# Performance work log

Hardware: AMD Instinct MI355X
Metric: run time of the kernel (lower is better)

The kernel has to match this reference:

```python
import jax, jax.numpy as jnp
import numpy as np

B, S, D = 2, 2048, 1024
H, HK, HD = 16, 4, 64          # query heads, kv heads, head dim = D//H
WIN = 1024                     # sliding attention window
E, K, DH = 8, 2, 2048          # experts, top_k, expert hidden (== d_head ctor arg)
ATTN_EPS, FFN_EPS = 1e-5, 1e-6
ROPE_THETA = 10000.0


def setup_inputs() -> dict:
    key = jax.random.key(0)
    ks = jax.random.split(key, 9)
    sc = 0.02
    # real rotary frequencies for positions [start_pos, start_pos+S)
    start_pos = 0
    inv_freq = 1.0 / (ROPE_THETA ** (jnp.arange(0, HD, 2, dtype=jnp.float32) / HD))  # [HD//2]
    pos = jnp.arange(start_pos, start_pos + S, dtype=jnp.float32)
    ang = pos[:, None] * inv_freq[None, :]  # [S, HD//2]
    return {
        'x': jax.random.normal(ks[0], (B, S, D), jnp.float32),
        'freqs_cos': jnp.cos(ang),
        'freqs_sin': jnp.sin(ang),
        'attn_norm_w': jnp.ones((D,), jnp.float32),
        'wq': jax.random.normal(ks[1], (D, H * HD), jnp.float32) * sc,
        'wk': jax.random.normal(ks[2], (D, HK * HD), jnp.float32) * sc,
        'wv': jax.random.normal(ks[3], (D, HK * HD), jnp.float32) * sc,
        'wo': jax.random.normal(ks[4], (H * HD, D), jnp.float32) * sc,
        'ffn_norm_w': jnp.ones((D,), jnp.float32),
        'router_w': jax.random.normal(ks[5], (D, E), jnp.float32) * sc,
        'w1': jax.random.normal(ks[6], (E, D, DH), jnp.float32) * sc,
        'w2': jax.random.normal(ks[7], (E, DH, D), jnp.float32) * sc,
        'start_pos': start_pos,
    }


def _rmsnorm(x, w, eps):
    return x * jax.lax.rsqrt(jnp.mean(x * x, axis=-1, keepdims=True) + eps) * w


def _rope(t, cos, sin):
    # t: [B,S,N,HD]; cos/sin: [S,HD//2] -> complex rotation on consecutive pairs
    shp = t.shape
    t = t.reshape(shp[:-1] + (HD // 2, 2))
    t0, t1 = t[..., 0], t[..., 1]
    c = cos[None, :, None, :]
    s = sin[None, :, None, :]
    r = jnp.stack([t0 * c - t1 * s, t0 * s + t1 * c], axis=-1)
    return r.reshape(shp)


def reference(x, freqs_cos, freqs_sin, attn_norm_w, wq, wk, wv, wo,
              ffn_norm_w, router_w, w1, w2, start_pos):
    # ---- attention sublayer (RMSNorm -> GQA sliding-window attn) ----
    hn = _rmsnorm(x, attn_norm_w, ATTN_EPS)
    q = (hn @ wq).reshape(B, S, H, HD)
    k = (hn @ wk).reshape(B, S, HK, HD)
    v = (hn @ wv).reshape(B, S, HK, HD)
    q = _rope(q, freqs_cos, freqs_sin)
    k = _rope(k, freqs_cos, freqs_sin)
    rep = H // HK
    k = jnp.repeat(k, rep, axis=2)  # [B,S,H,HD]
    v = jnp.repeat(v, rep, axis=2)
    scale = 1.0 / np.sqrt(HD).astype(np.float32)
    scores = jnp.einsum('bqhd,bkhd->bhqk', q, k) * scale  # [B,H,S,S]
    qi = jnp.arange(S) + start_pos
    kj = jnp.arange(S) + start_pos
    mask = (kj[None, :] <= qi[:, None]) & (qi[:, None] - kj[None, :] < WIN)
    scores = jnp.where(mask[None, None], scores, jnp.float32(-1e30))
    attn = jax.nn.softmax(scores, axis=-1)
    o = jnp.einsum('bhqk,bkhd->bqhd', attn, v).reshape(B, S, H * HD)
    h = x + o @ wo

    # ---- MoE sublayer (RMSNorm -> router top-k -> expert FFNs) ----
    fn = _rmsnorm(h, ffn_norm_w, FFN_EPS).reshape(-1, D)  # [T,D], T=B*S
    probs = jax.nn.softmax(fn @ router_w, axis=-1)        # [T,E]
    top_vals, top_idx = jax.lax.top_k(probs, K)           # [T,K]
    gates = top_vals / jnp.sum(top_vals, axis=-1, keepdims=True)
    gmat = jnp.sum(jax.nn.one_hot(top_idx, E, dtype=fn.dtype) * gates[..., None], axis=1)  # [T,E]
    moe = jnp.zeros_like(fn)
    for e in range(E):  # fixed small expert count
        moe = moe + gmat[:, e:e + 1] * (jax.nn.silu(fn @ w1[e]) @ w2[e])
    return h + moe.reshape(B, S, D)
```

## Files before the change

kernel.cpp:

```cpp
#include <hip/hip_runtime.h>
#include <hip/hip_bf16.h>

using bf16 = __hip_bfloat16;
typedef __attribute__((ext_vector_type(8))) short bf16x8;
typedef __attribute__((ext_vector_type(4))) short short4v;
typedef __attribute__((ext_vector_type(4))) float f32x4;

#define DEV static __device__ __forceinline__

DEV float b2f(bf16 v) { return __bfloat162float(v); }
DEV bf16  f2b(float f) { return __float2bfloat16(f); }
DEV short bbits(float f) { bf16 h = __float2bfloat16(f); short u; __builtin_memcpy(&u, &h, 2); return u; }

#define GL2LDS(g, l)                                                        \
  __builtin_amdgcn_global_load_lds(                                         \
      (const __attribute__((address_space(1))) void*)(g),                   \
      (__attribute__((address_space(3))) void*)(l), 16, 0, 0)

__global__ __launch_bounds__(256) void transpose_convert(
    const float* __restrict__ src, bf16* __restrict__ dst, int K, int N) {
  __shared__ float tile[64][65];
  int n0 = blockIdx.x * 64, k0 = blockIdx.y * 64;
  size_t bo = (size_t)blockIdx.z * K * N;
  src += bo; dst += bo;
  int t = threadIdx.x;
  int rr = t >> 4, cc = (t & 15) * 4;
#pragma unroll
  for (int p = 0; p < 4; ++p) {
    int r = rr + p * 16;
    const float4 v = *(const float4*)&src[(size_t)(k0 + r) * N + n0 + cc];
    tile[r][cc] = v.x; tile[r][cc + 1] = v.y; tile[r][cc + 2] = v.z; tile[r][cc + 3] = v.w;
  }
  __syncthreads();
#pragma unroll
  for (int p = 0; p < 4; ++p) {
    int nr = rr + p * 16;
    short4v o;
    o[0] = bbits(tile[cc + 0][nr]);
    o[1] = bbits(tile[cc + 1][nr]);
    o[2] = bbits(tile[cc + 2][nr]);
    o[3] = bbits(tile[cc + 3][nr]);
    *(short4v*)&dst[(size_t)(n0 + nr) * K + k0 + cc] = o;
  }
}

__global__ __launch_bounds__(256) void rmsnorm_kernel(
    const float* __restrict__ x, const float* __restrict__ w,
    bf16* __restrict__ o, float eps) {
  int row = blockIdx.x;
  const float* xr = x + (size_t)row * 1024;
  int t = threadIdx.x;
  float4 v = *(const float4*)&xr[t * 4];
  float ss = v.x * v.x + v.y * v.y + v.z * v.z + v.w * v.w;
#pragma unroll
  for (int d = 32; d; d >>= 1) ss += __shfl_down(ss, d);
  __shared__ float red[4];
  if ((t & 63) == 0) red[t >> 6] = ss;
  __syncthreads();
  float sum = red[0] + red[1] + red[2] + red[3];
  float sc = rsqrtf(sum * (1.f / 1024.f) + eps);
  const float4 wv = *(const float4*)&w[t * 4];
  short4v pk;
  pk[0] = bbits(v.x * sc * wv.x);
  pk[1] = bbits(v.y * sc * wv.y);
  pk[2] = bbits(v.z * sc * wv.z);
  pk[3] = bbits(v.w * sc * wv.w);
  *(short4v*)&o[(size_t)row * 1024 + t * 4] = pk;
}

__global__ __launch_bounds__(256) void rope_kernel(
    bf16* __restrict__ tbuf, const float* __restrict__ fcos,
    const float* __restrict__ fsin, int ncols, int pshift) {
  int tid = blockIdx.x * 256 + threadIdx.x;
  int row = tid >> pshift;
  int cp = tid & ((1 << pshift) - 1);
  if (row >= 4096) return;
  int i = cp & 31;
  int s = row & 2047;
  bf16* p = tbuf + (size_t)row * ncols + cp * 2;
  float t0 = b2f(p[0]), t1 = b2f(p[1]);
  float c = fcos[s * 32 + i], sn = fsin[s * 32 + i];
  p[0] = f2b(t0 * c - t1 * sn);
  p[1] = f2b(t0 * sn + t1 * c);
}

template <int MODE>
__global__ __launch_bounds__(256) void gemm_bt(
    const bf16* __restrict__ A, const bf16* __restrict__ Bt,
    int M, int N, int Kd,
    bf16* __restrict__ outb, float* __restrict__ outf,
    const float* __restrict__ resid,
    const int* __restrict__ counts, const int* __restrict__ offsets,
    const int* __restrict__ tok, const int* __restrict__ slotl,
    const float* __restrict__ gatel,
    float* __restrict__ slot0, float* __restrict__ slot1) {
  int count = M, off = 0;
  const bf16* Ap = A;
  const bf16* Bp = Bt;
  if (MODE == 2 || MODE == 3) {
    int e = blockIdx.z;
    count = counts[e]; off = offsets[e];
    Bp = Bt + (size_t)e * Kd * N;
    if (MODE == 3) Ap = A + (size_t)off * Kd;
  }
  int mb = blockIdx.y * 128, nb = blockIdx.x * 128;
  if (mb >= count) return;

  __shared__ __align__(16) bf16 As[2][128 * 32];
  __shared__ __align__(16) bf16 Bs[2][128 * 32];

  int t = threadIdx.x;
  int lane = t & 63, wid = t >> 6;

  const bf16* agl[2];
  const bf16* bgl[2];
#pragma unroll
  for (int iss = 0; iss < 2; ++iss) {
    int p = iss * 256 + wid * 64 + lane;
    int row = p >> 2, cs = p & 3;
    int c = cs ^ (row & 3);
    int m = mb + row;
    const bf16* abase;
    if (MODE == 2) {
      int tokid = (m < count) ? tok[off + m] : 0;
      abase = A + (size_t)tokid * Kd;
    } else {
      int mm = (m < count) ? m : 0;
      abase = Ap + (size_t)mm * Kd;
    }
    agl[iss] = abase + c * 8;
    bgl[iss] = Bp + (size_t)(nb + row) * Kd + c * 8;
  }

  int wr = (wid >> 1) * 64, wc = (wid & 1) * 64;
  int lr = lane & 15, lkc = lane >> 4;

  auto stage = [&](int buf, int kt) {
#pragma unroll
    for (int iss = 0; iss < 2; ++iss) {
      GL2LDS(agl[iss] + kt * 32, &As[buf][(iss * 256 + wid * 64) * 8]);
      GL2LDS(bgl[iss] + kt * 32, &Bs[buf][(iss * 256 + wid * 64) * 8]);
    }
  };

  const f32x4 fzero = {0.f, 0.f, 0.f, 0.f};
  f32x4 acc[4][4];
#pragma unroll
  for (int i = 0; i < 4; ++i)
#pragma unroll
    for (int j = 0; j < 4; ++j) acc[i][j] = fzero;

  int nk = Kd >> 5;
  stage(0, 0);
  __syncthreads();
  for (int kt = 0; kt < nk; ++kt) {
    int cur = kt & 1;
    if (kt + 1 < nk) stage(cur ^ 1, kt + 1);
    bf16x8 af[4], bfr[4];
#pragma unroll
    for (int i = 0; i < 4; ++i) {
      int r = wr + i * 16 + lr;
      af[i] = *(const bf16x8*)&As[cur][r * 32 + ((lkc ^ (r & 3)) * 8)];
    }
#pragma unroll
    for (int j = 0; j < 4; ++j) {
      int r = wc + j * 16 + lr;
      bfr[j] = *(const bf16x8*)&Bs[cur][r * 32 + ((lkc ^ (r & 3)) * 8)];
    }
#pragma unroll
    for (int i = 0; i < 4; ++i)
#pragma unroll
      for (int j = 0; j < 4; ++j)
        acc[i][j] = __builtin_amdgcn_mfma_f32_16x16x32_bf16(af[i], bfr[j], acc[i][j], 0, 0, 0);
    __syncthreads();
  }

  int rq = lane >> 4;
#pragma unroll
  for (int i = 0; i < 4; ++i) {
#pragma unroll
    for (int j = 0; j < 4; ++j) {
      if (MODE == 4) {
        int n = nb + wc + j * 16 + lr;
        int kh = n >> 6, d = n & 63;
        int m0 = mb + wr + i * 16 + rq * 4;
        int bb = m0 >> 11, s = m0 & 2047;
        short4v pk;
#pragma unroll
        for (int r = 0; r < 4; ++r) pk[r] = bbits(acc[i][j][r]);
        *(short4v*)&outb[((size_t)((bb * 4 + kh) * 64 + d)) * 2048 + s] = pk;
      } else {
#pragma unroll
        for (int r = 0; r < 4; ++r) {
          int m = mb + wr + i * 16 + rq * 4 + r;
          int n = nb + wc + j * 16 + lr;
          float v = acc[i][j][r];
          if (MODE == 0) {
            outb[(size_t)m * N + n] = f2b(v);
          } else if (MODE == 1) {
            outf[(size_t)m * N + n] = resid[(size_t)m * N + n] + v;
          } else if (MODE == 2) {
            if (m < count) {
              float sg = 1.f / (1.f + expf(-v));
              outb[(size_t)(off + m) * N + n] = f2b(v * sg);
            }
          } else if (MODE == 3) {
            if (m < count) {
              int row = off + m;
              int tk = tok[row];
              float g = gatel[row];
              float* dst = slotl[row] ? slot1 : slot0;
              dst[(size_t)tk * N + n] = g * v;
            }
          }
        }
      }
    }
  }
}

__global__ __launch_bounds__(256) void attn_kernel(
    const bf16* __restrict__ q, const bf16* __restrict__ kb,
    const bf16* __restrict__ vt, bf16* __restrict__ o) {
  int qb = blockIdx.x, h = blockIdx.y, b = blockIdx.z;
  int kh = h >> 2;
  int t = threadIdx.x;
  int lane = t & 63, wid = t >> 6;
  int lr = lane & 15, lkc = lane >> 4;
  int q0 = qb * 64;
  int qrow = q0 + wid * 16;

  __shared__ __align__(16) bf16 Ks[64 * 64];
  __shared__ __align__(16) bf16 Vs[64 * 64];
  __shared__ __align__(16) bf16 Ps[4][16 * 72];

  bf16x8 aq[2];
#pragma unroll
  for (int kk = 0; kk < 2; ++kk)
    aq[kk] = *(const bf16x8*)&q[(size_t)(b * 2048 + qrow + lr) * 1024 + h * 64 + kk * 32 + lkc * 8];

  const f32x4 fzero = {0.f, 0.f, 0.f, 0.f};
  f32x4 oacc[4];
  float mrun[4], lrun[4];
#pragma unroll
  for (int r = 0; r < 4; ++r) { oacc[r] = fzero; mrun[r] = -1e30f; lrun[r] = 0.f; }

  int klo = q0 - 1023; if (klo < 0) klo = 0;
  int tlo = klo >> 6, thi = q0 >> 6;
  int skey = t >> 3;
  int sch = t & 7;

  for (int kt = tlo; kt <= thi; ++kt) {
    int kbase = kt * 64;
#pragma unroll
    for (int pp = 0; pp < 2; ++pp) {
      int key = skey + pp * 32;
      bf16x8 kv = *(const bf16x8*)&kb[(size_t)(b * 2048 + kbase + key) * 256 + kh * 64 + sch * 8];
      *(bf16x8*)&Ks[key * 64 + ((sch ^ (key & 7)) * 8)] = kv;
      bf16x8 vv = *(const bf16x8*)&vt[((size_t)((b * 4 + kh) * 64 + key)) * 2048 + kbase + sch * 8];
      *(bf16x8*)&Vs[key * 64 + ((sch ^ (key & 7)) * 8)] = vv;
    }
    __syncthreads();

    f32x4 sacc[4];
#pragma unroll
    for (int nt = 0; nt < 4; ++nt) sacc[nt] = fzero;
#pragma unroll
    for (int nt = 0; nt < 4; ++nt)
#pragma unroll
      for (int kk = 0; kk < 2; ++kk) {
        int r = nt * 16 + lr;
        bf16x8 bk = *(const bf16x8*)&Ks[r * 64 + (((kk * 4 + lkc) ^ (r & 7)) * 8)];
        sacc[nt] = __builtin_amdgcn_mfma_f32_16x16x32_bf16(aq[kk], bk, sacc[nt], 0, 0, 0);
      }

    float sval[4][4], mt[4];
    int qg = qrow + lkc * 4;
#pragma unroll
    for (int r = 0; r < 4; ++r) mt[r] = -1e30f;
#pragma unroll
    for (int nt = 0; nt < 4; ++nt) {
      int kkey = kbase + nt * 16 + lr;
#pragma unroll
      for (int r = 0; r < 4; ++r) {
        float s = sacc[nt][r] * 0.125f;
        int qq = qg + r;
        bool valid = (kkey <= qq) && (qq - kkey < 1024);
        s = valid ? s : -1e30f;
        sval[nt][r] = s;
        mt[r] = fmaxf(mt[r], s);
      }
    }
#pragma unroll
    for (int d = 1; d < 16; d <<= 1)
#pragma unroll
      for (int r = 0; r < 4; ++r) mt[r] = fmaxf(mt[r], __shfl_xor(mt[r], d));
    float alpha[4], rs[4];
#pragma unroll
    for (int r = 0; r < 4; ++r) {
      float mn = fmaxf(mrun[r], mt[r]);
      alpha[r] = __expf(mrun[r] - mn);
      mrun[r] = mn;
      rs[r] = 0.f;
    }
#pragma unroll
    for (int nt = 0; nt < 4; ++nt)
#pragma unroll
      for (int r = 0; r < 4; ++r) {
        float pv = __expf(sval[nt][r] - mrun[r]);
        sval[nt][r] = pv;
        rs[r] += pv;
      }
#pragma unroll
    for (int d = 1; d < 16; d <<= 1)
#pragma unroll
      for (int r = 0; r < 4; ++r) rs[r] += __shfl_xor(rs[r], d);
#pragma unroll
    for (int r = 0; r < 4; ++r) lrun[r] = lrun[r] * alpha[r] + rs[r];
#pragma unroll
    for (int dt = 0; dt < 4; ++dt) {
      f32x4 t4 = oacc[dt];
#pragma unroll
      for (int r = 0; r < 4; ++r) t4[r] *= alpha[r];
      oacc[dt] = t4;
    }

    bf16* pw = &Ps[wid][0];
#pragma unroll
    for (int nt = 0; nt < 4; ++nt)
#pragma unroll
      for (int r = 0; r < 4; ++r)
        pw[(lkc * 4 + r) * 72 + nt * 16 + lr] = f2b(sval[nt][r]);
    __syncthreads();

    bf16x8 pa[2];
#pragma unroll
    for (int kk2 = 0; kk2 < 2; ++kk2)
      pa[kk2] = *(const bf16x8*)&pw[lr * 72 + kk2 * 32 + lkc * 8];
#pragma unroll
    for (int dt = 0; dt < 4; ++dt)
#pragma unroll
      for (int kk2 = 0; kk2 < 2; ++kk2) {
        int rrow = dt * 16 + lr;
        bf16x8 bv = *(const bf16x8*)&Vs[rrow * 64 + (((kk2 * 4 + lkc) ^ (rrow & 7)) * 8)];
        oacc[dt] = __builtin_amdgcn_mfma_f32_16x16x32_bf16(pa[kk2], bv, oacc[dt], 0, 0, 0);
      }
    __syncthreads();
  }

#pragma unroll
  for (int dt = 0; dt < 4; ++dt)
#pragma unroll
    for (int r = 0; r < 4; ++r) {
      int qq = qrow + lkc * 4 + r;
      int dd = dt * 16 + lr;
      o[(size_t)(b * 2048 + qq) * 1024 + h * 64 + dd] = f2b(oacc[dt][r] / lrun[r]);
    }
}

__global__ __launch_bounds__(256) void router_kernel(
    const float* __restrict__ h, const float* __restrict__ ffnw,
    const float* __restrict__ rw, float* __restrict__ gates,
    int* __restrict__ eidx) {
  int wid = threadIdx.x >> 6, lane = threadIdx.x & 63;
  int row = blockIdx.x * 4 + wid;
  const float* hr = h + (size_t)row * 1024;
  float xs[16];
  float ss = 0.f;
#pragma unroll
  for (int i = 0; i < 16; ++i) { float f = hr[lane + i * 64]; xs[i] = f; ss += f * f; }
#pragma unroll
  for (int d = 32; d; d >>= 1) ss += __shfl_xor(ss, d);
  float sc = rsqrtf(ss * (1.f / 1024.f) + 1e-6f);
  float lg[8];
#pragma unroll
  for (int e = 0; e < 8; ++e) lg[e] = 0.f;
#pragma unroll
  for (int i = 0; i < 16; ++i) {
    int d = lane + i * 64;
    float f = xs[i] * sc * ffnw[d];
    const float* rr = rw + d * 8;
#pragma unroll
    for (int e = 0; e < 8; ++e) lg[e] += f * rr[e];
  }
#pragma unroll
  for (int d = 32; d; d >>= 1)
#pragma unroll
    for (int e = 0; e < 8; ++e) lg[e] += __shfl_xor(lg[e], d);
  if (lane == 0) {
    int e0 = 0; float v0 = lg[0];
#pragma unroll
    for (int e = 1; e < 8; ++e) if (lg[e] > v0) { v0 = lg[e]; e0 = e; }
    int e1 = -1; float v1 = -1e30f;
#pragma unroll
    for (int e = 0; e < 8; ++e) if (e != e0 && lg[e] > v1) { v1 = lg[e]; e1 = e; }
    float r1 = expf(v1 - v0);
    float den = 1.f + r1;
    gates[row * 2] = 1.f / den;
    gates[row * 2 + 1] = r1 / den;
    eidx[row * 2] = e0;
    eidx[row * 2 + 1] = e1;
  }
}

__global__ __launch_bounds__(1024) void moe_setup(
    const int* __restrict__ eidx, const float* __restrict__ gates,
    int* __restrict__ counts, int* __restrict__ offsets,
    int* __restrict__ tok, int* __restrict__ slotl, float* __restrict__ gatel) {
  __shared__ int hist[8];
  __shared__ int cur[8];
  int t = threadIdx.x;
  if (t < 8) hist[t] = 0;
  __syncthreads();
  int e[8];
#pragma unroll
  for (int c = 0; c < 8; ++c) {
    e[c] = eidx[c * 1024 + t];
    atomicAdd(&hist[e[c]], 1);
  }
  __syncthreads();
  if (t == 0) {
    int o = 0;
#pragma unroll
    for (int i = 0; i < 8; ++i) {
      offsets[i] = o; cur[i] = o;
      int cnt = hist[i]; counts[i] = cnt; o += cnt;
    }
  }
  __syncthreads();
#pragma unroll
  for (int c = 0; c < 8; ++c) {
    int i = c * 1024 + t;
    int pos = atomicAdd(&cur[e[c]], 1);
    tok[pos] = i >> 1;
    slotl[pos] = i & 1;
    gatel[pos] = gates[i];
  }
}

__global__ __launch_bounds__(256) void final_add(
    const float* __restrict__ h, const float* __restrict__ s0,
    const float* __restrict__ s1, float* __restrict__ out) {
  size_t i = ((size_t)blockIdx.x * 256 + threadIdx.x) * 4;
  float4 a = *(const float4*)&h[i];
  float4 b = *(const float4*)&s0[i];
  float4 c = *(const float4*)&s1[i];
  float4 o;
  o.x = a.x + b.x + c.x; o.y = a.y + b.y + c.y;
  o.z = a.z + b.z + c.z; o.w = a.w + b.w + c.w;
  *(float4*)&out[i] = o;
}

extern "C" void kernel_launch(void* const* d_in, const int* in_sizes, int n_in,
                              void* d_out, int out_size, void* d_ws, size_t ws_size,
                              hipStream_t stream) {
  const float* x    = (const float*)d_in[0];
  const float* fcos = (const float*)d_in[1];
  const float* fsin = (const float*)d_in[2];
  const float* attw = (const float*)d_in[3];
  const float* wq   = (const float*)d_in[4];
  const float* wk   = (const float*)d_in[5];
  const float* wv   = (const float*)d_in[6];
  const float* wo   = (const float*)d_in[7];
  const float* ffnw = (const float*)d_in[8];
  const float* rw   = (const float*)d_in[9];
  const float* w1   = (const float*)d_in[10];
  const float* w2   = (const float*)d_in[11];
  float* out = (float*)d_out;

  const int M = 4096;
  char* p = (char*)d_ws;
  auto alloc = [&](size_t b) { char* r = p; p += (b + 255) & ~(size_t)255; return r; };

  bf16* hn    = (bf16*)alloc((size_t)M * 1024 * 2);
  bf16* qb    = (bf16*)alloc((size_t)M * 1024 * 2);
  bf16* kbuf  = (bf16*)alloc((size_t)M * 256 * 2);
  bf16* vt    = (bf16*)alloc((size_t)M * 256 * 2);
  bf16* ob    = (bf16*)alloc((size_t)M * 1024 * 2);
  float* hbuf = (float*)alloc((size_t)M * 1024 * 4);
  bf16* fn    = (bf16*)alloc((size_t)M * 1024 * 2);
  bf16* wqt   = (bf16*)alloc((size_t)1024 * 1024 * 2);
  bf16* wkt   = (bf16*)alloc((size_t)256 * 1024 * 2);
  bf16* wvt   = (bf16*)alloc((size_t)256 * 1024 * 2);
  bf16* wot   = (bf16*)alloc((size_t)1024 * 1024 * 2);
  bf16* w1t   = (bf16*)alloc((size_t)8 * 2048 * 1024 * 2);
  bf16* w2t   = (bf16*)alloc((size_t)8 * 1024 * 2048 * 2);
  bf16* act   = (bf16*)alloc((size_t)8192 * 2048 * 2);
  float* slot0 = (float*)alloc((size_t)M * 1024 * 4);
  float* slot1 = (float*)alloc((size_t)M * 1024 * 4);
  float* gates = (float*)alloc((size_t)M * 2 * 4);
  int* eidx    = (int*)alloc((size_t)M * 2 * 4);
  int* counts  = (int*)alloc(8 * 4);
  int* offsets = (int*)alloc(8 * 4);
  int* tok     = (int*)alloc(8192 * 4);
  int* slotl   = (int*)alloc(8192 * 4);
  float* gatel = (float*)alloc(8192 * 4);

  transpose_convert<<<dim3(16, 16, 1), 256, 0, stream>>>(wq, wqt, 1024, 1024);
  transpose_convert<<<dim3(4, 16, 1), 256, 0, stream>>>(wk, wkt, 1024, 256);
  transpose_convert<<<dim3(4, 16, 1), 256, 0, stream>>>(wv, wvt, 1024, 256);
  transpose_convert<<<dim3(16, 16, 1), 256, 0, stream>>>(wo, wot, 1024, 1024);
  transpose_convert<<<dim3(32, 16, 8), 256, 0, stream>>>(w1, w1t, 1024, 2048);
  transpose_convert<<<dim3(16, 32, 8), 256, 0, stream>>>(w2, w2t, 2048, 1024);

  rmsnorm_kernel<<<M, 256, 0, stream>>>(x, attw, hn, 1e-5f);

  gemm_bt<0><<<dim3(8, 32, 1), 256, 0, stream>>>(hn, wqt, M, 1024, 1024, qb, nullptr, nullptr,
      nullptr, nullptr, nullptr, nullptr, nullptr, nullptr, nullptr);
  gemm_bt<0><<<dim3(2, 32, 1), 256, 0, stream>>>(hn, wkt, M, 256, 1024, kbuf, nullptr, nullptr,
      nullptr, nullptr, nullptr, nullptr, nullptr, nullptr, nullptr);
  gemm_bt<4><<<dim3(2, 32, 1), 256, 0, stream>>>(hn, wvt, M, 256, 1024, vt, nullptr, nullptr,
      nullptr, nullptr, nullptr, nullptr, nullptr, nullptr, nullptr);

  rope_kernel<<<(M * 512) / 256, 256, 0, stream>>>(qb, fcos, fsin, 1024, 9);
  rope_kernel<<<(M * 128) / 256, 256, 0, stream>>>(kbuf, fcos, fsin, 256, 7);

  attn_kernel<<<dim3(32, 16, 2), 256, 0, stream>>>(qb, kbuf, vt, ob);

  gemm_bt<1><<<dim3(8, 32, 1), 256, 0, stream>>>(ob, wot, M, 1024, 1024, nullptr, hbuf, x,
      nullptr, nullptr, nullptr, nullptr, nullptr, nullptr, nullptr);

  rmsnorm_kernel<<<M, 256, 0, stream>>>(hbuf, ffnw, fn, 1e-6f);

  router_kernel<<<M / 4, 256, 0, stream>>>(hbuf, ffnw, rw, gates, eidx);
  moe_setup<<<1, 1024, 0, stream>>>(eidx, gates, counts, offsets, tok, slotl, gatel);

  gemm_bt<2><<<dim3(16, 32, 8), 256, 0, stream>>>(fn, w1t, M, 2048, 1024, act, nullptr, nullptr,
      counts, offsets, tok, nullptr, nullptr, nullptr, nullptr);
  gemm_bt<3><<<dim3(8, 32, 8), 256, 0, stream>>>(act, w2t, M, 1024, 2048, nullptr, nullptr, nullptr,
      counts, offsets, tok, slotl, gatel, slot0, slot1);

  final_add<<<M, 256, 0, stream>>>(hbuf, slot0, slot1, out);
}
```

Before: 402.3 us.

## Write expert outputs as contiguous bf16 and gather via inverse index in final add

```diff
diff --git a/kernel.cpp b/kernel.cpp
--- a/kernel.cpp
+++ b/kernel.cpp
@@ -11,6 +11,10 @@
 DEV float b2f(bf16 v) { return __bfloat162float(v); }
 DEV bf16  f2b(float f) { return __float2bfloat16(f); }
 DEV short bbits(float f) { bf16 h = __float2bfloat16(f); short u; __builtin_memcpy(&u, &h, 2); return u; }
+DEV float sb2f(short s) {
+  unsigned u = ((unsigned)(unsigned short)s) << 16;
+  float f; __builtin_memcpy(&f, &u, 4); return f;
+}
 
 #define GL2LDS(g, l)                                                        \
   __builtin_amdgcn_global_load_lds(                                         \
@@ -91,9 +95,7 @@
     bf16* __restrict__ outb, float* __restrict__ outf,
     const float* __restrict__ resid,
     const int* __restrict__ counts, const int* __restrict__ offsets,
-    const int* __restrict__ tok, const int* __restrict__ slotl,
-    const float* __restrict__ gatel,
-    float* __restrict__ slot0, float* __restrict__ slot1) {
+    const int* __restrict__ tok, const float* __restrict__ gatel) {
   int count = M, off = 0;
   const bf16* Ap = A;
   const bf16* Bp = Bt;
@@ -103,7 +105,11 @@
     Bp = Bt + (size_t)e * Kd * N;
     if (MODE == 3) Ap = A + (size_t)off * Kd;
   }
-  int mb = blockIdx.y * 128, nb = blockIdx.x * 128;
+  int gx = gridDim.x;
+  int flat = blockIdx.y * gx + blockIdx.x;
+  int cpx = (gx * gridDim.y) >> 3;
+  int swz = (flat & 7) * cpx + (flat >> 3);
+  int mb = (swz / gx) * 128, nb = (swz % gx) * 128;
   if (mb >= count) return;
 
   __shared__ __align__(16) bf16 As[2][128 * 32];
@@ -207,10 +213,7 @@
           } else if (MODE == 3) {
             if (m < count) {
               int row = off + m;
-              int tk = tok[row];
-              float g = gatel[row];
-              float* dst = slotl[row] ? slot1 : slot0;
-              dst[(size_t)tk * N + n] = g * v;
+              outb[(size_t)row * N + n] = f2b(gatel[row] * v);
             }
           }
         }
@@ -406,7 +409,7 @@
 __global__ __launch_bounds__(1024) void moe_setup(
     const int* __restrict__ eidx, const float* __restrict__ gates,
     int* __restrict__ counts, int* __restrict__ offsets,
-    int* __restrict__ tok, int* __restrict__ slotl, float* __restrict__ gatel) {
+    int* __restrict__ tok, float* __restrict__ gatel, int* __restrict__ inv) {
   __shared__ int hist[8];
   __shared__ int cur[8];
   int t = threadIdx.x;
@@ -433,22 +436,27 @@
     int i = c * 1024 + t;
     int pos = atomicAdd(&cur[e[c]], 1);
     tok[pos] = i >> 1;
-    slotl[pos] = i & 1;
     gatel[pos] = gates[i];
+    inv[i] = pos;
   }
 }
 
 __global__ __launch_bounds__(256) void final_add(
-    const float* __restrict__ h, const float* __restrict__ s0,
-    const float* __restrict__ s1, float* __restrict__ out) {
-  size_t i = ((size_t)blockIdx.x * 256 + threadIdx.x) * 4;
-  float4 a = *(const float4*)&h[i];
-  float4 b = *(const float4*)&s0[i];
-  float4 c = *(const float4*)&s1[i];
+    const float* __restrict__ h, const bf16* __restrict__ y2,
+    const int* __restrict__ inv, float* __restrict__ out) {
+  int tokid = blockIdx.x;
+  int t = threadIdx.x;
+  int i0 = inv[tokid * 2], i1 = inv[tokid * 2 + 1];
+  size_t base = (size_t)tokid * 1024 + t * 4;
+  float4 a = *(const float4*)&h[base];
+  short4v p0 = *(const short4v*)&y2[(size_t)i0 * 1024 + t * 4];
+  short4v p1 = *(const short4v*)&y2[(size_t)i1 * 1024 + t * 4];
   float4 o;
-  o.x = a.x + b.x + c.x; o.y = a.y + b.y + c.y;
-  o.z = a.z + b.z + c.z; o.w = a.w + b.w + c.w;
-  *(float4*)&out[i] = o;
+  o.x = a.x + sb2f(p0[0]) + sb2f(p1[0]);
+  o.y = a.y + sb2f(p0[1]) + sb2f(p1[1]);
+  o.z = a.z + sb2f(p0[2]) + sb2f(p1[2]);
+  o.w = a.w + sb2f(p0[3]) + sb2f(p1[3]);
+  *(float4*)&out[base] = o;
 }
 
 extern "C" void kernel_launch(void* const* d_in, const int* in_sizes, int n_in,
@@ -486,14 +494,13 @@
   bf16* w1t   = (bf16*)alloc((size_t)8 * 2048 * 1024 * 2);
   bf16* w2t   = (bf16*)alloc((size_t)8 * 1024 * 2048 * 2);
   bf16* act   = (bf16*)alloc((size_t)8192 * 2048 * 2);
-  float* slot0 = (float*)alloc((size_t)M * 1024 * 4);
-  float* slot1 = (float*)alloc((size_t)M * 1024 * 4);
+  bf16* y2    = (bf16*)alloc((size_t)8192 * 1024 * 2);
   float* gates = (float*)alloc((size_t)M * 2 * 4);
   int* eidx    = (int*)alloc((size_t)M * 2 * 4);
   int* counts  = (int*)alloc(8 * 4);
   int* offsets = (int*)alloc(8 * 4);
   int* tok     = (int*)alloc(8192 * 4);
-  int* slotl   = (int*)alloc(8192 * 4);
+  int* inv     = (int*)alloc(8192 * 4);
   float* gatel = (float*)alloc(8192 * 4);
 
   transpose_convert<<<dim3(16, 16, 1), 256, 0, stream>>>(wq, wqt, 1024, 1024);
@@ -506,11 +513,11 @@
   rmsnorm_kernel<<<M, 256, 0, stream>>>(x, attw, hn, 1e-5f);
 
   gemm_bt<0><<<dim3(8, 32, 1), 256, 0, stream>>>(hn, wqt, M, 1024, 1024, qb, nullptr, nullptr,
-      nullptr, nullptr, nullptr, nullptr, nullptr, nullptr, nullptr);
+      nullptr, nullptr, nullptr, nullptr);
   gemm_bt<0><<<dim3(2, 32, 1), 256, 0, stream>>>(hn, wkt, M, 256, 1024, kbuf, nullptr, nullptr,
-      nullptr, nullptr, nullptr, nullptr, nullptr, nullptr, nullptr);
+      nullptr, nullptr, nullptr, nullptr);
   gemm_bt<4><<<dim3(2, 32, 1), 256, 0, stream>>>(hn, wvt, M, 256, 1024, vt, nullptr, nullptr,
-      nullptr, nullptr, nullptr, nullptr, nullptr, nullptr, nullptr);
+      nullptr, nullptr, nullptr, nullptr);
 
   rope_kernel<<<(M * 512) / 256, 256, 0, stream>>>(qb, fcos, fsin, 1024, 9);
   rope_kernel<<<(M * 128) / 256, 256, 0, stream>>>(kbuf, fcos, fsin, 256, 7);
@@ -518,17 +525,17 @@
   attn_kernel<<<dim3(32, 16, 2), 256, 0, stream>>>(qb, kbuf, vt, ob);
 
   gemm_bt<1><<<dim3(8, 32, 1), 256, 0, stream>>>(ob, wot, M, 1024, 1024, nullptr, hbuf, x,
-      nullptr, nullptr, nullptr, nullptr, nullptr, nullptr, nullptr);
+      nullptr, nullptr, nullptr, nullptr);
 
   rmsnorm_kernel<<<M, 256, 0, stream>>>(hbuf, ffnw, fn, 1e-6f);
 
   router_kernel<<<M / 4, 256, 0, stream>>>(hbuf, ffnw, rw, gates, eidx);
-  moe_setup<<<1, 1024, 0, stream>>>(eidx, gates, counts, offsets, tok, slotl, gatel);
-
-  gemm_bt<2><<<dim3(16, 32, 8), 256, 0, stream>>>(fn, w1t, M, 2048, 1024, act, nullptr, nullptr,
-      counts, offsets, tok, nullptr, nullptr, nullptr, nullptr);
-  gemm_bt<3><<<dim3(8, 32, 8), 256, 0, stream>>>(act, w2t, M, 1024, 2048, nullptr, nullptr, nullptr,
-      counts, offsets, tok, slotl, gatel, slot0, slot1);
-
-  final_add<<<M, 256, 0, stream>>>(hbuf, slot0, slot1, out);
-}
+  moe_setup<<<1, 1024, 0, stream>>>(eidx, gates, counts, offsets, tok, gatel, inv);
+
+  gemm_bt<2><<<dim3(16, 64, 8), 256, 0, stream>>>(fn, w1t, M, 2048, 1024, act, nullptr, nullptr,
+      counts, offsets, tok, nullptr);
+  gemm_bt<3><<<dim3(8, 64, 8), 256, 0, stream>>>(act, w2t, M, 1024, 2048, y2, nullptr, nullptr,
+      counts, offsets, tok, gatel);
+
+  final_add<<<M, 256, 0, stream>>>(hbuf, y2, inv, out);
+}
```

After: 975.0 us. +142.4%, slower.
